# Optimization experiments

Measured on AMD Instinct MI355X. Metric: run time of the kernel, lower is better.

The kernel has to match this reference:

```python
import jax, jax.numpy as jnp
import numpy as np

B, H, W = 32, 128, 128
NA = 9            # number of anchors
STRIDE = 16.0
CLS_THRESH = 0.95
MAX_IOU = 0.1
NUM_PROP = 10
NEG = -1e9        # sentinel for suppressed / below-threshold scores


def setup_inputs() -> dict:
    key = jax.random.key(0)
    inputs = jax.random.normal(key, (B, H, W, NA * 4 + NA + 1), dtype=jnp.float32)
    anchors = jnp.array([[0.5, 32.0], [1.0, 32.0], [2.0, 32.0],
                         [0.5, 64.0], [1.0, 64.0], [2.0, 64.0],
                         [0.5, 128.0], [1.0, 128.0], [2.0, 128.0]], dtype=jnp.float32)
    return {"inputs": inputs, "anchors": anchors}


def _decode(inputs, anchors):
    b, h, w, c = inputs.shape
    cls = inputs[..., -1]
    # zero out 1-pixel border (the tf.pad'ed cancel matrix)
    border = jnp.zeros((h, w), inputs.dtype).at[1:-1, 1:-1].set(1.0)
    cls = cls * border
    a_reg = inputs[..., -10:-1]           # [B,H,W,9]
    bbox_reg = inputs[..., :-10]          # [B,H,W,36]
    a_idx = jnp.argmax(a_reg, axis=-1)    # [B,H,W] best anchor per position
    # gather the 4 deltas of the chosen anchor: channels a_idx*4 .. a_idx*4+3
    gidx = a_idx[..., None] * 4 + jnp.arange(4)
    deltas = jnp.take_along_axis(bbox_reg, gidx, axis=-1)          # [B,H,W,4]
    anc = anchors[a_idx].astype(jnp.float32)                       # [B,H,W,2]
    # anchor box: center x from column, center y from row, height=anc[:,1], width=anc[:,1]/anc[:,0]
    ax = (jnp.arange(w, dtype=jnp.float32)[None, :] + 0.5) * STRIDE  # [1,W]
    ay = (jnp.arange(h, dtype=jnp.float32)[:, None] + 0.5) * STRIDE  # [H,1]
    a0 = jnp.broadcast_to(ax, (h, w))[None]                          # [1,H,W]
    a1 = jnp.broadcast_to(ay, (h, w))[None]
    a2 = anc[..., 1]
    a3 = anc[..., 1] / anc[..., 0]
    b0 = deltas[..., 0] * a2 + a0
    b1 = deltas[..., 1] * a3 + a1
    b2 = jnp.exp(deltas[..., 2]) * a2
    b3 = jnp.exp(deltas[..., 3]) * a3
    bboxes = jnp.stack([b0, b1, b2, b3], axis=-1)                    # [B,H,W,4]
    coords = jnp.stack([b1 - b3 / 2, b0 - b2 / 2,
                        b1 + b3 / 2, b0 + b2 / 2], axis=-1)          # [y1,x1,y2,x2]
    scores = jnp.where(cls > CLS_THRESH, cls, NEG)                   # mask below-threshold
    n = h * w
    return (bboxes.reshape(b, n, 4), coords.reshape(b, n, 4), scores.reshape(b, n))


def _nms_one(boxes, coords, scores):
    # greedy NMS, equivalent to tf.image.non_max_suppression over the valid candidates
    n = scores.shape[0]
    area = jnp.maximum(coords[:, 2] - coords[:, 0], 0.0) * jnp.maximum(coords[:, 3] - coords[:, 1], 0.0)
    idx_range = jnp.arange(n)

    def body(i, state):
        sc, out = state
        j = jnp.argmax(sc)
        ok = sc[j] > NEG / 2
        sel = coords[j]
        iy1 = jnp.maximum(coords[:, 0], sel[0])
        ix1 = jnp.maximum(coords[:, 1], sel[1])
        iy2 = jnp.minimum(coords[:, 2], sel[2])
        ix2 = jnp.minimum(coords[:, 3], sel[3])
        inter = jnp.maximum(iy2 - iy1, 0.0) * jnp.maximum(ix2 - ix1, 0.0)
        area_s = jnp.maximum(sel[2] - sel[0], 0.0) * jnp.maximum(sel[3] - sel[1], 0.0)
        iou = inter / (area + area_s - inter + 1e-10)
        suppress = (iou > MAX_IOU) | (idx_range == j)
        sc = jnp.where(ok & suppress, NEG, sc)
        out = out.at[i].set(jnp.where(ok, boxes[j], jnp.zeros(4, boxes.dtype)))
        return sc, out

    out0 = jnp.zeros((NUM_PROP, 4), boxes.dtype)
    _, out = jax.lax.fori_loop(0, NUM_PROP, body, (scores, out0))
    return out


def _forward(inputs, anchors):
    bboxes, coords, scores = _decode(inputs, anchors)
    return jax.vmap(_nms_one)(bboxes, coords, scores)   # [B, NUM_PROP, 4]


def reference(inputs, anchors):
    return _forward(inputs, anchors)
```

## Files before the change

kernel.cpp:

```cpp
#include <hip/hip_runtime.h>
#include <math.h>

#define BB 32
#define HH 128
#define WW 128
#define NA 9
#define CCH 46
#define NPIX (HH*WW)
#define STRIDE_F 16.0f
#define CLS_T 0.95f
#define MAX_IOU_F 0.1f
#define NUM_PROP 10
#define NEGV -1000000000.0f

#define TILE_PIX 256
#define TILE_FLOATS (TILE_PIX * CCH)
#define TILE_VEC (TILE_FLOATS / 4)

#define NTILE (BB * NPIX / TILE_PIX)
#define NWAVES (NTILE * 4)
#define WSLOT 64

#define NMS_T 512
#define MAXPER 10
#define MMAX (MAXPER * NMS_T)

#define GLL16(gp, lp)                                                          \
  __builtin_amdgcn_global_load_lds(                                            \
      (__attribute__((address_space(1))) void*)(gp),                           \
      (__attribute__((address_space(3))) void*)(lp), 16, 0, 0)

__global__ __launch_bounds__(256, 3) void decode_kernel(
    const float* __restrict__ in, const float* __restrict__ anchors,
    int* __restrict__ wcnt, float* __restrict__ sc_comp,
    float4* __restrict__ co_comp)
{
  __shared__ float s_in[TILE_FLOATS];

  int tid = threadIdx.x;
  int tile = blockIdx.x;
  int g0 = tile * TILE_PIX;

  const float4* srcv = (const float4*)(in + (size_t)g0 * CCH);
  float4* dstv = (float4*)s_in;
#pragma unroll
  for (int i = 0; i < 12; ++i) {
    int k = tid + i * 256;
    if (k < TILE_VEC)
      GLL16(srcv + k, dstv + k);
  }
  __syncthreads();

  int g = g0 + tid;
  int p = g & (NPIX - 1);
  int h = p >> 7;
  int w = p & (WW - 1);
  const float* px = s_in + tid * CCH;

  float cls = px[45];
  bool interior = (h >= 1) && (h <= HH - 2) && (w >= 1) && (w <= WW - 2);
  bool cand = interior && (cls > CLS_T);

  unsigned long long mask = __ballot(cand);
  int lane = tid & 63;
  int waveid = tile * 4 + (tid >> 6);
  int total = __popcll(mask);
  if (lane == 0) wcnt[waveid] = total;

  if (!cand) return;

  int ai = 0; float av = px[36];
#pragma unroll
  for (int c = 1; c < NA; ++c) { float v = px[36 + c]; if (v > av) { av = v; ai = c; } }

  float d0 = px[ai * 4 + 0], d1 = px[ai * 4 + 1];
  float d2 = px[ai * 4 + 2], d3 = px[ai * 4 + 3];
  float ratio = anchors[ai * 2 + 0], sz = anchors[ai * 2 + 1];
  float a2 = sz, a3 = sz / ratio;
  float ax = ((float)w + 0.5f) * STRIDE_F;
  float ay = ((float)h + 0.5f) * STRIDE_F;
  float b0 = d0 * a2 + ax;
  float b1 = d1 * a3 + ay;
  float b2 = expf(d2) * a2;
  float b3 = expf(d3) * a3;
  float4 co = make_float4(b1 - 0.5f * b3, b0 - 0.5f * b2,
                          b1 + 0.5f * b3, b0 + 0.5f * b2);

  int prefix = __popcll(mask & ((1ull << lane) - 1ull));
  int slot = waveid * WSLOT + prefix;
  sc_comp[slot] = cls;
  co_comp[slot] = co;
}

__global__ __launch_bounds__(NMS_T, 1) void nms_kernel(
    const int* __restrict__ wcnt, const float* __restrict__ sc_comp,
    const float4* __restrict__ co_comp, float* __restrict__ out)
{
  __shared__ int    s_pref[256];
  __shared__ int    s_wtot[4];
  __shared__ float  s_rv[2][8];
  __shared__ int    s_rk[2][8];
  __shared__ float4 s_rc[2][8];

  int b = blockIdx.x, tid = threadIdx.x;
  int lane = tid & 63, wv = tid >> 6;

  int c = (tid < 256) ? wcnt[b * 256 + tid] : 0;
  int v = c;
#pragma unroll
  for (int off = 1; off < 64; off <<= 1) {
    int u = __shfl_up(v, off);
    if (lane >= off) v += u;
  }
  if (wv < 4 && lane == 63) s_wtot[wv] = v;
  __syncthreads();
  int add = 0;
#pragma unroll
  for (int q = 0; q < 3; ++q) if (q < wv) add += s_wtot[q];
  if (tid < 256) s_pref[tid] = v + add;
  __syncthreads();
  int M = s_pref[255];
  if (M > MMAX) M = MMAX;

  float  sc[MAXPER];
  float4 co[MAXPER];
  float  ar[MAXPER];
#pragma unroll
  for (int r = 0; r < MAXPER; ++r) {
    int k = r * NMS_T + tid;
    if (k < M) {
      int lo = 0, hi = 255;
#pragma unroll
      for (int s = 0; s < 8; ++s) {
        int mid = (lo + hi) >> 1;
        if (s_pref[mid] > k) hi = mid; else lo = mid + 1;
      }
      int excl = (lo > 0) ? s_pref[lo - 1] : 0;
      size_t base = (size_t)(b * 256 + lo) * WSLOT + (k - excl);
      sc[r] = sc_comp[base];
      co[r] = co_comp[base];
      ar[r] = fmaxf(co[r].z - co[r].x, 0.f) * fmaxf(co[r].w - co[r].y, 0.f);
    } else {
      sc[r] = NEGV; co[r] = make_float4(0.f, 0.f, 0.f, 0.f); ar[r] = 0.f;
    }
  }

  int buf = 0;
  for (int it = 0; it < NUM_PROP; ++it) {
    float bv = -INFINITY; int bk = 0x7fffffff;
    float4 bc = make_float4(0.f, 0.f, 0.f, 0.f);
#pragma unroll
    for (int r = 0; r < MAXPER; ++r) {
      if (sc[r] > bv) { bv = sc[r]; bk = r * NMS_T + tid; bc = co[r]; }
    }
#pragma unroll
    for (int off = 32; off > 0; off >>= 1) {
      float ov  = __shfl_down(bv, off);
      int   ok_ = __shfl_down(bk, off);
      float ox  = __shfl_down(bc.x, off);
      float oy  = __shfl_down(bc.y, off);
      float oz  = __shfl_down(bc.z, off);
      float ow  = __shfl_down(bc.w, off);
      if (ov > bv || (ov == bv && ok_ < bk)) {
        bv = ov; bk = ok_; bc = make_float4(ox, oy, oz, ow);
      }
    }
    if (lane == 0) { s_rv[buf][wv] = bv; s_rk[buf][wv] = bk; s_rc[buf][wv] = bc; }
    __syncthreads();
    float jv = s_rv[buf][0]; int jk = s_rk[buf][0]; float4 jc = s_rc[buf][0];
#pragma unroll
    for (int q = 1; q < 8; ++q) {
      float qv = s_rv[buf][q]; int qk = s_rk[buf][q];
      if (qv > jv || (qv == jv && qk < jk)) { jv = qv; jk = qk; jc = s_rc[buf][q]; }
    }
    buf ^= 1;

    bool okq = jv > (NEGV * 0.5f);
    if (okq) {
      float sy1 = jc.x, sx1 = jc.y, sy2 = jc.z, sx2 = jc.w;
      float sarea = fmaxf(sy2 - sy1, 0.f) * fmaxf(sx2 - sx1, 0.f);
#pragma unroll
      for (int r = 0; r < MAXPER; ++r) {
        float4 cc = co[r];
        float iy1 = fmaxf(cc.x, sy1);
        float ix1 = fmaxf(cc.y, sx1);
        float iy2 = fminf(cc.z, sy2);
        float ix2 = fminf(cc.w, sx2);
        float inter = fmaxf(iy2 - iy1, 0.f) * fmaxf(ix2 - ix1, 0.f);
        float iou = inter / (ar[r] + sarea - inter + 1e-10f);
        if (iou > MAX_IOU_F || (r * NMS_T + tid) == jk) sc[r] = NEGV;
      }
      if (tid == 0) {
        float* o = out + (size_t)(b * NUM_PROP + it) * 4;
        o[0] = 0.5f * (sx1 + sx2);
        o[1] = 0.5f * (sy1 + sy2);
        o[2] = sx2 - sx1;
        o[3] = sy2 - sy1;
      }
    } else {
      if (tid == 0) {
        for (int it2 = it; it2 < NUM_PROP; ++it2) {
          float* o = out + (size_t)(b * NUM_PROP + it2) * 4;
          o[0] = 0.f; o[1] = 0.f; o[2] = 0.f; o[3] = 0.f;
        }
      }
      break;
    }
  }
}

extern "C" void kernel_launch(void* const* d_in, const int* in_sizes, int n_in,
                              void* d_out, int out_size, void* d_ws, size_t ws_size,
                              hipStream_t stream) {
  const float* in      = (const float*)d_in[0];
  const float* anchors = (const float*)d_in[1];
  float* out = (float*)d_out;

  char* ws = (char*)d_ws;
  int*    wcnt    = (int*)ws;
  float4* co_comp = (float4*)(ws + (size_t)NWAVES * 4);
  float*  sc_comp = (float*)(ws + (size_t)NWAVES * 4 + (size_t)NWAVES * WSLOT * 16);

  decode_kernel<<<NTILE, 256, 0, stream>>>(in, anchors, wcnt, sc_comp, co_comp);
  nms_kernel<<<BB, NMS_T, 0, stream>>>(wcnt, sc_comp, co_comp, out);
}
```

Measured before the change: 171.9 us.

## Read only score and anchor-logit channels directly instead of staging full tile in LDS

The decode kernel no longer copies every 46-channel pixel record into shared memory. Each thread now loads only channels 36–45 from global memory as float2 vectors, and only threads whose pixel passes the threshold fetch the four deltas of the chosen anchor. The LDS buffer and its barrier are removed, and the occupancy hint is raised. The aim is to cut global traffic and LDS pressure, at the cost of strided, partially coalesced per-thread loads.

Measured after the change: 173.0 us. Within noise of the previous version (+0.6%).

```diff
diff --git a/kernel.cpp b/kernel.cpp
--- a/kernel.cpp
+++ b/kernel.cpp
@@ -13,76 +13,62 @@
 #define NUM_PROP 10
 #define NEGV -1000000000.0f
 
-#define TILE_PIX 256
-#define TILE_FLOATS (TILE_PIX * CCH)
-#define TILE_VEC (TILE_FLOATS / 4)
-
-#define NTILE (BB * NPIX / TILE_PIX)
-#define NWAVES (NTILE * 4)
+#define NTHR 256
+#define NBLK (BB * NPIX / NTHR)
+#define NWAVES (NBLK * 4)
 #define WSLOT 64
 
 #define NMS_T 512
 #define MAXPER 10
 #define MMAX (MAXPER * NMS_T)
 
-#define GLL16(gp, lp)                                                          \
-  __builtin_amdgcn_global_load_lds(                                            \
-      (__attribute__((address_space(1))) void*)(gp),                           \
-      (__attribute__((address_space(3))) void*)(lp), 16, 0, 0)
-
-__global__ __launch_bounds__(256, 3) void decode_kernel(
+__global__ __launch_bounds__(NTHR, 4) void decode_kernel(
     const float* __restrict__ in, const float* __restrict__ anchors,
     int* __restrict__ wcnt, float* __restrict__ sc_comp,
     float4* __restrict__ co_comp)
 {
-  __shared__ float s_in[TILE_FLOATS];
-
   int tid = threadIdx.x;
-  int tile = blockIdx.x;
-  int g0 = tile * TILE_PIX;
-
-  const float4* srcv = (const float4*)(in + (size_t)g0 * CCH);
-  float4* dstv = (float4*)s_in;
-#pragma unroll
-  for (int i = 0; i < 12; ++i) {
-    int k = tid + i * 256;
-    if (k < TILE_VEC)
-      GLL16(srcv + k, dstv + k);
-  }
-  __syncthreads();
-
-  int g = g0 + tid;
+  int g = blockIdx.x * NTHR + tid;
   int p = g & (NPIX - 1);
   int h = p >> 7;
   int w = p & (WW - 1);
-  const float* px = s_in + tid * CCH;
-
-  float cls = px[45];
+
+  const float* rec = in + (size_t)g * CCH;
+  const float2* lp = (const float2*)(rec + 36);
+  float2 l0 = lp[0];
+  float2 l1 = lp[1];
+  float2 l2 = lp[2];
+  float2 l3 = lp[3];
+  float2 l4 = lp[4];
+
+  float cls = l4.y;
   bool interior = (h >= 1) && (h <= HH - 2) && (w >= 1) && (w <= WW - 2);
   bool cand = interior && (cls > CLS_T);
 
   unsigned long long mask = __ballot(cand);
   int lane = tid & 63;
-  int waveid = tile * 4 + (tid >> 6);
-  int total = __popcll(mask);
-  if (lane == 0) wcnt[waveid] = total;
+  int waveid = blockIdx.x * 4 + (tid >> 6);
+  if (lane == 0) wcnt[waveid] = __popcll(mask);
 
   if (!cand) return;
 
-  int ai = 0; float av = px[36];
-#pragma unroll
-  for (int c = 1; c < NA; ++c) { float v = px[36 + c]; if (v > av) { av = v; ai = c; } }
-
-  float d0 = px[ai * 4 + 0], d1 = px[ai * 4 + 1];
-  float d2 = px[ai * 4 + 2], d3 = px[ai * 4 + 3];
+  float lg[9] = { l0.x, l0.y, l1.x, l1.y, l2.x, l2.y, l3.x, l3.y, l4.x };
+  int ai = 0; float av = lg[0];
+#pragma unroll
+  for (int c = 1; c < NA; ++c) { if (lg[c] > av) { av = lg[c]; ai = c; } }
+
+  const float2* dp = (const float2*)(rec + ai * 4);
+  float2 d01 = dp[0];
+  float2 d23 = dp[1];
+
   float ratio = anchors[ai * 2 + 0], sz = anchors[ai * 2 + 1];
   float a2 = sz, a3 = sz / ratio;
   float ax = ((float)w + 0.5f) * STRIDE_F;
   float ay = ((float)h + 0.5f) * STRIDE_F;
-  float b0 = d0 * a2 + ax;
-  float b1 = d1 * a3 + ay;
-  float b2 = expf(d2) * a2;
-  float b3 = expf(d3) * a3;
+  float b0 = d01.x * a2 + ax;
+  float b1 = d01.y * a3 + ay;
+  float b2 = expf(d23.x) * a2;
+  float b3 = expf(d23.y) * a3;
   float4 co = make_float4(b1 - 0.5f * b3, b0 - 0.5f * b2,
                           b1 + 0.5f * b3, b0 + 0.5f * b2);
 
@@ -221,6 +207,6 @@
   float4* co_comp = (float4*)(ws + (size_t)NWAVES * 4);
   float*  sc_comp = (float*)(ws + (size_t)NWAVES * 4 + (size_t)NWAVES * WSLOT * 16);
 
-  decode_kernel<<<NTILE, 256, 0, stream>>>(in, anchors, wcnt, sc_comp, co_comp);
+  decode_kernel<<<NBLK, NTHR, 0, stream>>>(in, anchors, wcnt, sc_comp, co_comp);
   nms_kernel<<<BB, NMS_T, 0, stream>>>(wcnt, sc_comp, co_comp, out);
 }
```
